# Optimization experiments

Measured on AMD Instinct MI355X. Metric: run time of the kernel, lower is better.

## Reference

```python
import jax, jax.numpy as jnp
import numpy as np

KS = 3      # deformable kernel size
PAD = 1     # module padding


def conv3x3(x, w, b):
    y = jax.lax.conv_general_dilated(
        x, w, window_strides=(1, 1), padding=((1, 1), (1, 1)),
        dimension_numbers=('NCHW', 'OIHW', 'NCHW'))
    return y + b[None, :, None, None]


def setup_inputs() -> dict:
    key = jax.random.key(0)
    ks = jax.random.split(key, 9)
    B, C, H, W = 4, 64, 128, 128
    f = lambda k, s: jax.random.normal(k, s, dtype=jnp.float32)
    return {
        'feature_size': f(ks[0], (B, C, H, W)),
        'feature_context': f(ks[1], (B, C, H, W)),
        'x': f(ks[2], (B, C, H, W)),
        'p_conv_w': f(ks[3], (2 * KS * KS, C, 3, 3)) * 0.01,
        'p_conv_b': f(ks[4], (2 * KS * KS,)) * 0.01,
        'f_conv_w': f(ks[5], (C * KS * KS, C, 3, 3)) * 0.05,
        'f_conv_b': f(ks[6], (C * KS * KS,)) * 0.05,
        'm_conv_w': f(ks[7], (KS * KS, C, 3, 3)) * 0.01,
        'm_conv_b': f(ks[8], (KS * KS,)) * 0.01,
    }


def reference(feature_size, feature_context, x,
              p_conv_w, p_conv_b, f_conv_w, f_conv_b, m_conv_w, m_conv_b):
    ks = KS
    N = ks * ks
    offset = conv3x3(feature_size, p_conv_w, p_conv_b)            # [B, 2N, H, W]
    psffilter = conv3x3(feature_context, f_conv_w, f_conv_b)      # [B, C*N, H, W]
    m = jax.nn.sigmoid(conv3x3(feature_size, m_conv_w, m_conv_b)) # [B, N, H, W]

    B, C, H, W = x.shape
    xp = jnp.pad(x, ((0, 0), (0, 0), (PAD, PAD), (PAD, PAD)))     # [B, C, H+2, W+2]
    Hp, Wp = xp.shape[2], xp.shape[3]

    # sampling locations p = p0 + pn + offset (coords in padded frame; p0 starts at 1)
    r = jnp.arange(-(ks - 1) // 2, (ks - 1) // 2 + 1, dtype=jnp.float32)
    dx = jnp.repeat(r, ks)        # rows:  [-1,-1,-1, 0,0,0, 1,1,1]
    dy = jnp.tile(r, ks)          # cols:  [-1, 0, 1] * 3
    pn = jnp.concatenate([dx, dy])[None, :, None, None]           # [1, 2N, 1, 1]
    px0 = jnp.arange(1, H + 1, dtype=jnp.float32)[None, None, :, None]
    py0 = jnp.arange(1, W + 1, dtype=jnp.float32)[None, None, None, :]
    p0 = jnp.concatenate([jnp.broadcast_to(px0, (1, N, H, W)),
                          jnp.broadcast_to(py0, (1, N, H, W))], axis=1)
    p = jnp.transpose(p0 + pn + offset, (0, 2, 3, 1))             # [B, H, W, 2N]
    px, py = p[..., :N], p[..., N:]

    fx, fy = jnp.floor(px), jnp.floor(py)
    ltx = jnp.clip(fx, 0, Hp - 1)
    lty = jnp.clip(fy, 0, Wp - 1)
    rbx = jnp.clip(fx + 1, 0, Hp - 1)
    rby = jnp.clip(fy + 1, 0, Wp - 1)
    pxc = jnp.clip(px, 0, Hp - 1)
    pyc = jnp.clip(py, 0, Wp - 1)

    g_lt = (1 + (ltx - pxc)) * (1 + (lty - pyc))
    g_rb = (1 - (rbx - pxc)) * (1 - (rby - pyc))
    g_lb = (1 + (ltx - pxc)) * (1 - (rby - pyc))
    g_rt = (1 - (rbx - pxc)) * (1 + (lty - pyc))

    ltx_i, lty_i = ltx.astype(jnp.int32), lty.astype(jnp.int32)
    rbx_i, rby_i = rbx.astype(jnp.int32), rby.astype(jnp.int32)

    gather = jax.vmap(lambda xb, ix, iy: xb[:, ix, iy])  # per-batch -> [C, H, W, N]
    x_lt = gather(xp, ltx_i, lty_i)
    x_rb = gather(xp, rbx_i, rby_i)
    x_lb = gather(xp, ltx_i, rby_i)
    x_rt = gather(xp, rbx_i, lty_i)

    x_off = (g_lt[:, None] * x_lt + g_rb[:, None] * x_rb +
             g_lb[:, None] * x_lb + g_rt[:, None] * x_rt)         # [B, C, H, W, N]

    x_off = x_off * jnp.transpose(m, (0, 2, 3, 1))[:, None]       # modulation

    # _reshape_x_offset: [B,C,H,W,ks,ks] -> [B,C,H*ks,W*ks]
    x_off = x_off.reshape(B, C, H, W, ks, ks)
    x_off = x_off.transpose(0, 1, 2, 4, 3, 5).reshape(B, C, H * ks, W * ks)

    # FAC: unfold(kernel=ks, stride=ks, pad=(ks-1)//2) then per-pixel filter mult-sum
    pad = (ks - 1) // 2
    xf = jnp.pad(x_off, ((0, 0), (0, 0), (pad, pad), (pad, pad)))
    xf = xf[:, :, :H * ks, :W * ks].reshape(B, C, H, ks, W, ks)
    xf = xf.transpose(0, 2, 4, 1, 3, 5).reshape(B, H, W, C, ks * ks)   # [B,H,W,C,9]
    weight = jnp.transpose(psffilter, (0, 2, 3, 1)).reshape(B, H, W, C, ks * ks)
    out = jnp.einsum('bhwck,bhwck->bchw', xf, weight)
    return out
```

## Files before the change

kernel.cpp:

```cpp
#include <hip/hip_runtime.h>

typedef __bf16 bf16;
typedef __bf16 bf16x8 __attribute__((ext_vector_type(8)));
typedef unsigned short u16x8 __attribute__((ext_vector_type(8)));
typedef float f32x4 __attribute__((ext_vector_type(4)));
typedef int i32x4 __attribute__((ext_vector_type(4)));

#define HH 128
#define WW 128
#define HP 130

__global__ __launch_bounds__(256) void zero_rings(
    bf16* __restrict__ fs_t, bf16* __restrict__ ctx_t, float* __restrict__ xp) {
  const int idx = blockIdx.x * 256 + threadIdx.x;
  const f32x4 z = {0.f, 0.f, 0.f, 0.f};
  int r, chunk;
  char* base;
  if (idx < 33024) {
    chunk = idx & 7;
    int cell = idx >> 3;
    r = cell % 516;
    int bb = cell / 516;
    int b = bb & 3;
    bf16* out = (bb >> 2) ? ctx_t : fs_t;
    int row, col;
    if (r < 130)      { row = 0;   col = r; }
    else if (r < 260) { row = 129; col = r - 130; }
    else { int s = r - 260; row = 1 + (s >> 1); col = (s & 1) ? 129 : 0; }
    base = (char*)(out + ((size_t)(b * HP + row) * HP + col) * 64);
  } else {
    int i2 = idx - 33024;
    chunk = i2 & 15;
    int cell = i2 >> 4;
    r = cell % 516;
    int b = cell / 516;
    int row, col;
    if (r < 130)      { row = 0;   col = r; }
    else if (r < 260) { row = 129; col = r - 130; }
    else { int s = r - 260; row = 1 + (s >> 1); col = (s & 1) ? 129 : 0; }
    base = (char*)(xp + ((size_t)(b * HP + row) * HP + col) * 64);
  }
  *reinterpret_cast<f32x4*>(base + chunk * 16) = z;
}

__global__ __launch_bounds__(256) void transpose_all(
    const float* __restrict__ fs, const float* __restrict__ ctx,
    const float* __restrict__ x, bf16* __restrict__ fs_t,
    bf16* __restrict__ ctx_t, float* __restrict__ xp) {
  __shared__ float tile[64][65];
  const int z = blockIdx.z;
  const int b = z & 3, which = z >> 2;
  const float* in = which == 0 ? fs : (which == 1 ? ctx : x);
  const int y = blockIdx.y, x0 = blockIdx.x * 64;
  const int tid = threadIdx.x;
#pragma unroll
  for (int pass = 0; pass < 16; ++pass) {
    int ci = pass * 4 + (tid >> 6), xx = tid & 63;
    tile[ci][xx] = in[((b * 64 + ci) * HH + y) * WW + x0 + xx];
  }
  __syncthreads();
  if (which == 2) {
#pragma unroll
    for (int pass = 0; pass < 16; ++pass) {
      int xx = pass * 4 + (tid >> 6), ci = tid & 63;
      xp[((size_t)(b * HP + y + 1) * HP + (x0 + xx + 1)) * 64 + ci] = tile[ci][xx];
    }
  } else {
    bf16* out = which ? ctx_t : fs_t;
#pragma unroll
    for (int pass = 0; pass < 16; ++pass) {
      int xx = pass * 4 + (tid >> 6), ci = tid & 63;
      out[((size_t)(b * HP + y + 1) * HP + (x0 + xx + 1)) * 64 + ci] = (bf16)tile[ci][xx];
    }
  }
}

__global__ void build_bfrag(const float* __restrict__ fw,
                            const float* __restrict__ pw,
                            const float* __restrict__ mw,
                            bf16* __restrict__ dstPsf,
                            bf16* __restrict__ dstOffm) {
  if ((int)blockIdx.x < 162) {
    int idx = blockIdx.x * 256 + threadIdx.x;
    int lane = idx & 63;
    int nt = (idx >> 6) % 9;
    int kc = ((idx >> 6) / 9) % 18;
    int cc = (idx >> 6) / 162;
    int np = cc * 144 + nt * 16 + (lane & 15);
    int n = (np & 63) * 9 + (np >> 6);
    int q = lane >> 4;
    bf16x8 v;
#pragma unroll
    for (int j = 0; j < 8; ++j) {
      int k = kc * 32 + q * 8 + j;
      int tap = k >> 6, ci = k & 63;
      v[j] = (bf16)fw[(n * 64 + ci) * 9 + tap];
    }
    *reinterpret_cast<bf16x8*>(dstPsf + (size_t)idx * 8) = v;
  } else {
    int idx = (blockIdx.x - 162) * 256 + threadIdx.x;
    int lane = idx & 63;
    int nt = (idx >> 6) & 1;
    int kc = (idx >> 6) >> 1;
    int n = nt * 16 + (lane & 15);
    int q = lane >> 4;
    bf16x8 v;
#pragma unroll
    for (int j = 0; j < 8; ++j) {
      int k = kc * 32 + q * 8 + j;
      int tap = k >> 6, ci = k & 63;
      float w = 0.f;
      if (n < 18) w = pw[(n * 64 + ci) * 9 + tap];
      else if (n < 27) w = mw[((n - 18) * 64 + ci) * 9 + tap];
      v[j] = (bf16)w;
    }
    *reinterpret_cast<bf16x8*>(dstOffm + (size_t)idx * 8) = v;
  }
}

__global__ __launch_bounds__(512, 4) void conv_mega(
    const bf16* __restrict__ ctx_t, const bf16* __restrict__ fs_t,
    const bf16* __restrict__ Bf, const bf16* __restrict__ Bf2,
    const float* __restrict__ fb, const float* __restrict__ pb,
    const float* __restrict__ mb, bf16* __restrict__ Pg,
    float* __restrict__ OM, int b0, int offmN) {
  __shared__ __align__(16) char smem[78336];
  ushort* apatch = (ushort*)smem;
  const int tid = threadIdx.x;
  const int lane = tid & 63, wv = tid >> 6;
  const int q = lane >> 4, col = lane & 15;
  const int bid = blockIdx.x;

  if ((int)bid < offmN) {
    const int b = bid >> 6, t = bid & 63;
    const int h0 = (t >> 3) * 16, w0 = (t & 7) * 16;
    const ushort* Atu = (const ushort*)fs_t;
#pragma unroll
    for (int it = 0; it < 6; ++it) {
      int flat = it * 512 + tid;
      if (flat < 2592) {
        int px = flat >> 3, c8 = flat & 7;
        int py = px / 18, pxx = px - py * 18;
        u16x8 v = *(const u16x8*)(Atu + ((size_t)((b * HP + h0 + py) * HP + (w0 + pxx))) * 64 + c8 * 8);
        *(u16x8*)(apatch + px * 64 + ((c8 ^ (px & 7)) * 8)) = v;
      }
    }
    __syncthreads();
    f32x4 acc[2][2];
#pragma unroll
    for (int s = 0; s < 2; ++s) {
      acc[s][0] = (f32x4){0.f, 0.f, 0.f, 0.f};
      acc[s][1] = (f32x4){0.f, 0.f, 0.f, 0.f};
    }
    const bf16* bl = Bf2 + lane * 8;
#pragma unroll
    for (int dh = 0; dh < 3; ++dh)
#pragma unroll
      for (int dw = 0; dw < 3; ++dw) {
        const int tap = dh * 3 + dw;
        bf16x8 a[2][2];
#pragma unroll
        for (int s = 0; s < 2; ++s) {
          int p = (s * 8 + wv + dh) * 18 + (col + dw);
#pragma unroll
          for (int hf = 0; hf < 2; ++hf) {
            int ch = (hf * 4 + q) ^ (p & 7);
            a[s][hf] = *(const bf16x8*)((const bf16*)apatch + p * 64 + ch * 8);
          }
        }
#pragma unroll
        for (int hf = 0; hf < 2; ++hf)
#pragma unroll
          for (int nt = 0; nt < 2; ++nt) {
            bf16x8 bb = *(const bf16x8*)(bl + (size_t)(((tap * 2 + hf) * 2 + nt) * 512));
#pragma unroll
            for (int s = 0; s < 2; ++s)
              acc[s][nt] = __builtin_amdgcn_mfma_f32_16x16x32_bf16(a[s][hf], bb, acc[s][nt], 0, 0, 0);
          }
      }
    float* OMb = OM + (size_t)b * 16384 * 32;
#pragma unroll
    for (int nt = 0; nt < 2; ++nt) {
      int n = nt * 16 + col;
#pragma unroll
      for (int s = 0; s < 2; ++s) {
        int h = h0 + s * 8 + wv;
#pragma unroll
        for (int j = 0; j < 4; ++j) {
          int w = w0 + q * 4 + j;
          float v = acc[s][nt][j];
          float r;
          if (n < 18) r = v + pb[n];
          else if (n < 27) { float z = v + mb[n - 18]; r = 1.f / (1.f + __expf(-z)); }
          else r = 0.f;
          OMb[(size_t)(h * WW + w) * 32 + n] = r;
        }
      }
    }
    return;
  }

  const int pid = bid - offmN;
  const int cc = pid & 3;
  const int rest = pid >> 2;
  const int brel = rest >> 6;
  const int b = b0 + brel;
  const int t = rest & 63;
  const int h0 = (t >> 3) * 16, w0 = (t & 7) * 16;
  char* BsmBase = smem + 41472;
  const char* BfC = (const char*)Bf + (size_t)cc * 165888;

  {
    const char* gs = BfC;
#pragma unroll
    for (int it = 0; it < 3; ++it) {
      int flat = it * 512 + wv * 64;
      if (flat < 1152) {
        __builtin_amdgcn_global_load_lds(
            (const __attribute__((address_space(1))) void*)(gs + (size_t)(flat + lane) * 16),
            (__attribute__((address_space(3))) void*)(BsmBase + flat * 16), 16, 0, 0);
      }
    }
  }

  const ushort* Atu = (const ushort*)ctx_t;
#pragma unroll
  for (int it = 0; it < 6; ++it) {
    int flat = it * 512 + tid;
    if (flat < 2592) {
      int px = flat >> 3, c8 = flat & 7;
      int py = px / 18, pxx = px - py * 18;
      u16x8 v = *(const u16x8*)(Atu + ((size_t)((b * HP + h0 + py) * HP + (w0 + pxx))) * 64 + c8 * 8);
      *(u16x8*)(apatch + px * 64 + ((c8 ^ (px & 7)) * 8)) = v;
    }
  }
  __syncthreads();

  f32x4 acc[2][9];
#pragma unroll
  for (int s = 0; s < 2; ++s)
#pragma unroll
    for (int n = 0; n < 9; ++n) acc[s][n] = (f32x4){0.f, 0.f, 0.f, 0.f};

  for (int tap = 0; tap < 9; ++tap) {
    const int cur = tap & 1;
    if (tap < 8) {
      const char* gs = BfC + (tap + 1) * 18432;
      char* ld = BsmBase + (cur ^ 1) * 18432;
#pragma unroll
      for (int it = 0; it < 3; ++it) {
        int flat = it * 512 + wv * 64;
        if (flat < 1152) {
          __builtin_amdgcn_global_load_lds(
              (const __attribute__((address_space(1))) void*)(gs + (size_t)(flat + lane) * 16),
              (__attribute__((address_space(3))) void*)(ld + flat * 16), 16, 0, 0);
        }
      }
    }

    const int dh = tap >= 6 ? 2 : (tap >= 3 ? 1 : 0);
    const int dw = tap - dh * 3;
    bf16x8 a[2][2];
#pragma unroll
    for (int s = 0; s < 2; ++s) {
      int p = (s * 8 + wv + dh) * 18 + (col + dw);
#pragma unroll
      for (int hf = 0; hf < 2; ++hf) {
        int ch = (hf * 4 + q) ^ (p & 7);
        a[s][hf] = *(const bf16x8*)((const bf16*)apatch + p * 64 + ch * 8);
      }
    }
    const bf16* Bsm = (const bf16*)(BsmBase + cur * 18432);
#pragma unroll
    for (int hf = 0; hf < 2; ++hf) {
      const bf16* bp = Bsm + (size_t)(hf * 9) * 512 + lane * 8;
#pragma unroll
      for (int nt = 0; nt < 9; ++nt) {
        bf16x8 bb = *(const bf16x8*)(bp + nt * 512);
#pragma unroll
        for (int s = 0; s < 2; ++s)
          acc[s][nt] = __builtin_amdgcn_mfma_f32_16x16x32_bf16(a[s][hf], bb, acc[s][nt], 0, 0, 0);
      }
    }
    __syncthreads();
  }

  bf16* Pp = Pg + (size_t)brel * 16384 * 576;
#pragma unroll
  for (int nt = 0; nt < 9; ++nt) {
    int np = cc * 144 + nt * 16 + col;
    float bias = fb[(np & 63) * 9 + (np >> 6)];
#pragma unroll
    for (int s = 0; s < 2; ++s) {
      int h = h0 + s * 8 + wv;
#pragma unroll
      for (int j = 0; j < 4; ++j) {
        int w = w0 + q * 4 + j;
        Pp[(size_t)(h * WW + w) * 576 + np] = (bf16)(acc[s][nt][j] + bias);
      }
    }
  }
}

__global__ __launch_bounds__(256, 4) void sampler(
    const bf16* __restrict__ Pg, const float* __restrict__ xp,
    const float* __restrict__ OM, float* __restrict__ out, int b0) {
  __shared__ float smem[64][21];
  __shared__ __align__(16) float wts[144][4];
  __shared__ __align__(16) int   offs[144][4];
  const int tid = threadIdx.x;
  const int wv = tid >> 6, c = tid & 63;
  const int blk = blockIdx.x;
  const int brel = blk >> 10;
  const int b = b0 + brel;
  const int h = (blk >> 3) & 127;
  const int w0 = (blk & 7) * 16;

  const float* xpb = xp + (size_t)b * (HP * HP * 64) + c;
  const float* OMb = OM + (size_t)b * 16384 * 32;
  const bf16* Pbase = Pg + ((size_t)brel * 16384 + h * WW + w0) * 576;

  if (tid < 144) {
    const int pl = tid / 9, tap = tid - pl * 9;
    const int i3 = tap / 3, j3 = tap - i3 * 3;
    const int dh = (i3 == 0) ? -1 : 0, ri = (i3 == 0) ? 2 : (i3 - 1);
    const int dw = (j3 == 0) ? -1 : 0, rj = (j3 == 0) ? 2 : (j3 - 1);
    const int hh = h + dh, ww2 = w0 + pl + dw;
    f32x4 g = {0.f, 0.f, 0.f, 0.f};
    i32x4 o = {0, 0, 0, 0};
    if (hh >= 0 && ww2 >= 0) {
      const int np = ri * 3 + rj;
      const float* omp = OMb + (size_t)(hh * WW + ww2) * 32;
      float ox = omp[np], oy = omp[9 + np], mv = omp[18 + np];
      float px = (float)(hh + ri) + ox;
      float py = (float)(ww2 + rj) + oy;
      float fx = floorf(px), fy = floorf(py);
      float ltx = fminf(fmaxf(fx, 0.f), 129.f);
      float lty = fminf(fmaxf(fy, 0.f), 129.f);
      float rbx = fminf(fmaxf(fx + 1.f, 0.f), 129.f);
      float rby = fminf(fmaxf(fy + 1.f, 0.f), 129.f);
      float pxc = fminf(fmaxf(px, 0.f), 129.f);
      float pyc = fminf(fmaxf(py, 0.f), 129.f);
      g[0] = (1.f + ltx - pxc) * (1.f + lty - pyc) * mv;
      g[1] = (1.f - rbx + pxc) * (1.f - rby + pyc) * mv;
      g[2] = (1.f + ltx - pxc) * (1.f - rby + pyc) * mv;
      g[3] = (1.f - rbx + pxc) * (1.f + lty - pyc) * mv;
      int ix0 = (int)ltx, iy0 = (int)lty, ix1 = (int)rbx, iy1 = (int)rby;
      o[0] = (ix0 * HP + iy0) * 64;
      o[1] = (ix1 * HP + iy1) * 64;
      o[2] = (ix0 * HP + iy1) * 64;
      o[3] = (ix1 * HP + iy0) * 64;
    }
    *reinterpret_cast<f32x4*>(&wts[tid][0]) = g;
    *reinterpret_cast<i32x4*>(&offs[tid][0]) = o;
  }
  __syncthreads();

#pragma unroll
  for (int k = 0; k < 4; ++k) {
    const int pl = wv * 4 + k;
    const int w = w0 + pl;
    const bf16* Pp = Pbase + (size_t)pl * 576;
    float res = 0.f;
#pragma unroll
    for (int tap = 0; tap < 9; ++tap) {
      const int i3 = tap / 3, j3 = tap - i3 * 3;
      if ((i3 == 0 && h == 0) || (j3 == 0 && w == 0)) continue;
      const int idx = pl * 9 + tap;
      f32x4 g = *reinterpret_cast<const f32x4*>(&wts[idx][0]);
      i32x4 o = *reinterpret_cast<const i32x4*>(&offs[idx][0]);
      float x_lt = xpb[o[0]];
      float x_rb = xpb[o[1]];
      float x_lb = xpb[o[2]];
      float x_rt = xpb[o[3]];
      float sv = g[0] * x_lt + g[1] * x_rb + g[2] * x_lb + g[3] * x_rt;
      float pv = (float)Pp[tap * 64 + c];
      res += pv * sv;
    }
    smem[c][pl] = res;
  }
  __syncthreads();
  const int c2 = tid >> 2;
  const int wi = (tid & 3) * 4;
  f32x4 v;
#pragma unroll
  for (int i = 0; i < 4; ++i) v[i] = smem[c2][wi + i];
  *reinterpret_cast<f32x4*>(out + ((size_t)(b * 64 + c2) * HH + h) * WW + w0 + wi) = v;
}

extern "C" void kernel_launch(void* const* d_in, const int* in_sizes, int n_in,
                              void* d_out, int out_size, void* d_ws, size_t ws_size,
                              hipStream_t stream) {
  (void)in_sizes; (void)n_in; (void)out_size;
  const float* fs  = (const float*)d_in[0];
  const float* ctx = (const float*)d_in[1];
  const float* x   = (const float*)d_in[2];
  const float* pw  = (const float*)d_in[3];
  const float* pb  = (const float*)d_in[4];
  const float* fw  = (const float*)d_in[5];
  const float* fb  = (const float*)d_in[6];
  const float* mw  = (const float*)d_in[7];
  const float* mb  = (const float*)d_in[8];

  char* ws = (char*)d_ws;
  bf16*  ctx_t = (bf16*)(ws);
  bf16*  fs_t  = (bf16*)(ws + 8652800);
  float* xp    = (float*)(ws + 17305600);
  bf16*  Bf    = (bf16*)(ws + 34611200);
  bf16*  Bf2   = (bf16*)(ws + 35274752);
  float* OM    = (float*)(ws + 35311616);
  bf16*  Pg    = (bf16*)(ws + 43700224);

  zero_rings<<<258, 256, 0, stream>>>(fs_t, ctx_t, xp);
  transpose_all<<<dim3(2, 128, 12), 256, 0, stream>>>(fs, ctx, x, fs_t, ctx_t, xp);
  build_bfrag<<<171, 256, 0, stream>>>(fw, pw, mw, Bf, Bf2);

  const size_t need4 = 43700224 + 4ull * 18874368;
  if (ws_size >= need4) {
    conv_mega<<<1280, 512, 0, stream>>>(ctx_t, fs_t, Bf, Bf2, fb, pb, mb, Pg, OM, 0, 256);
    sampler<<<4096, 256, 0, stream>>>(Pg, xp, OM, (float*)d_out, 0);
  } else {
    conv_mega<<<768, 512, 0, stream>>>(ctx_t, fs_t, Bf, Bf2, fb, pb, mb, Pg, OM, 0, 256);
    sampler<<<2048, 256, 0, stream>>>(Pg, xp, OM, (float*)d_out, 0);
    conv_mega<<<512, 512, 0, stream>>>(ctx_t, fs_t, Bf, Bf2, fb, pb, mb, Pg, OM, 2, 0);
    sampler<<<2048, 256, 0, stream>>>(Pg, xp, OM, (float*)d_out, 2);
  }
}
```

Baseline: 190.0 us.

## Merge prep kernels into one launch and retile conv MFMA warp work 4x5

Three small preprocessing kernels (ring zeroing, transpose, B-fragment build) are folded into one launch whose block index selects the role, removing two launch gaps. In the main conv kernel, each wave now covers 4 pixel rows by 5 (or 4) N-tiles instead of 2 rows by all 9 N-tiles. This gives more A-fragment reuse per B load and fewer LDS B reads per MFMA. The accumulator footprint rises from 18 to 20 tiles, so launch bounds drop to 3 blocks per CU. The N split is uneven across wave groups, 5 vs 4 tiles, which leaves some imbalance.

```diff
diff --git a/kernel.cpp b/kernel.cpp
--- a/kernel.cpp
+++ b/kernel.cpp
@@ -10,78 +10,81 @@
 #define WW 128
 #define HP 130
 
-__global__ __launch_bounds__(256) void zero_rings(
-    bf16* __restrict__ fs_t, bf16* __restrict__ ctx_t, float* __restrict__ xp) {
-  const int idx = blockIdx.x * 256 + threadIdx.x;
-  const f32x4 z = {0.f, 0.f, 0.f, 0.f};
-  int r, chunk;
-  char* base;
-  if (idx < 33024) {
-    chunk = idx & 7;
-    int cell = idx >> 3;
-    r = cell % 516;
-    int bb = cell / 516;
-    int b = bb & 3;
-    bf16* out = (bb >> 2) ? ctx_t : fs_t;
-    int row, col;
-    if (r < 130)      { row = 0;   col = r; }
-    else if (r < 260) { row = 129; col = r - 130; }
-    else { int s = r - 260; row = 1 + (s >> 1); col = (s & 1) ? 129 : 0; }
-    base = (char*)(out + ((size_t)(b * HP + row) * HP + col) * 64);
-  } else {
-    int i2 = idx - 33024;
-    chunk = i2 & 15;
-    int cell = i2 >> 4;
-    r = cell % 516;
-    int b = cell / 516;
-    int row, col;
-    if (r < 130)      { row = 0;   col = r; }
-    else if (r < 260) { row = 129; col = r - 130; }
-    else { int s = r - 260; row = 1 + (s >> 1); col = (s & 1) ? 129 : 0; }
-    base = (char*)(xp + ((size_t)(b * HP + row) * HP + col) * 64);
-  }
-  *reinterpret_cast<f32x4*>(base + chunk * 16) = z;
-}
-
-__global__ __launch_bounds__(256) void transpose_all(
+__global__ __launch_bounds__(256) void prep(
     const float* __restrict__ fs, const float* __restrict__ ctx,
-    const float* __restrict__ x, bf16* __restrict__ fs_t,
-    bf16* __restrict__ ctx_t, float* __restrict__ xp) {
+    const float* __restrict__ x, const float* __restrict__ fw,
+    const float* __restrict__ pw, const float* __restrict__ mw,
+    bf16* __restrict__ fs_t, bf16* __restrict__ ctx_t, float* __restrict__ xp,
+    bf16* __restrict__ dstPsf, bf16* __restrict__ dstOffm) {
   __shared__ float tile[64][65];
-  const int z = blockIdx.z;
-  const int b = z & 3, which = z >> 2;
-  const float* in = which == 0 ? fs : (which == 1 ? ctx : x);
-  const int y = blockIdx.y, x0 = blockIdx.x * 64;
+  const int bid = blockIdx.x;
   const int tid = threadIdx.x;
-#pragma unroll
-  for (int pass = 0; pass < 16; ++pass) {
-    int ci = pass * 4 + (tid >> 6), xx = tid & 63;
-    tile[ci][xx] = in[((b * 64 + ci) * HH + y) * WW + x0 + xx];
-  }
-  __syncthreads();
-  if (which == 2) {
+
+  if (bid < 258) {
+    const int idx = bid * 256 + tid;
+    const f32x4 z = {0.f, 0.f, 0.f, 0.f};
+    int r, chunk;
+    char* base;
+    if (idx < 33024) {
+      chunk = idx & 7;
+      int cell = idx >> 3;
+      r = cell % 516;
+      int bb = cell / 516;
+      int b = bb & 3;
+      bf16* out = (bb >> 2) ? ctx_t : fs_t;
+      int row, col;
+      if (r < 130)      { row = 0;   col = r; }
+      else if (r < 260) { row = 129; col = r - 130; }
+      else { int s = r - 260; row = 1 + (s >> 1); col = (s & 1) ? 129 : 0; }
+      base = (char*)(out + ((size_t)(b * HP + row) * HP + col) * 64);
+    } else {
+      int i2 = idx - 33024;
+      chunk = i2 & 15;
+      int cell = i2 >> 4;
+      r = cell % 516;
+      int b = cell / 516;
+      int row, col;
+      if (r < 130)      { row = 0;   col = r; }
+      else if (r < 260) { row = 129; col = r - 130; }
+      else { int s = r - 260; row = 1 + (s >> 1); col = (s & 1) ? 129 : 0; }
+      base = (char*)(xp + ((size_t)(b * HP + row) * HP + col) * 64);
+    }
+    *reinterpret_cast<f32x4*>(base + chunk * 16) = z;
+    return;
+  }
+
+  if (bid < 3330) {
+    const int t = bid - 258;
+    const int bx = t & 1, by = (t >> 1) & 127, bz = t >> 8;
+    const int b = bz & 3, which = bz >> 2;
+    const float* in = which == 0 ? fs : (which == 1 ? ctx : x);
+    const int y = by, x0 = bx * 64;
 #pragma unroll
     for (int pass = 0; pass < 16; ++pass) {
-      int xx = pass * 4 + (tid >> 6), ci = tid & 63;
-      xp[((size_t)(b * HP + y + 1) * HP + (x0 + xx + 1)) * 64 + ci] = tile[ci][xx];
-    }
-  } else {
-    bf16* out = which ? ctx_t : fs_t;
-#pragma unroll
-    for (int pass = 0; pass < 16; ++pass) {
-      int xx = pass * 4 + (tid >> 6), ci = tid & 63;
-      out[((size_t)(b * HP + y + 1) * HP + (x0 + xx + 1)) * 64 + ci] = (bf16)tile[ci][xx];
-    }
-  }
-}
-
-__global__ void build_bfrag(const float* __restrict__ fw,
-                            const float* __restrict__ pw,
-                            const float* __restrict__ mw,
-                            bf16* __restrict__ dstPsf,
-                            bf16* __restrict__ dstOffm) {
-  if ((int)blockIdx.x < 162) {
-    int idx = blockIdx.x * 256 + threadIdx.x;
+      int ci = pass * 4 + (tid >> 6), xx = tid & 63;
+      tile[ci][xx] = in[((b * 64 + ci) * HH + y) * WW + x0 + xx];
+    }
+    __syncthreads();
+    if (which == 2) {
+#pragma unroll
+      for (int pass = 0; pass < 16; ++pass) {
+        int xx = pass * 4 + (tid >> 6), ci = tid & 63;
+        xp[((size_t)(b * HP + y + 1) * HP + (x0 + xx + 1)) * 64 + ci] = tile[ci][xx];
+      }
+    } else {
+      bf16* out = which ? ctx_t : fs_t;
+#pragma unroll
+      for (int pass = 0; pass < 16; ++pass) {
+        int xx = pass * 4 + (tid >> 6), ci = tid & 63;
+        out[((size_t)(b * HP + y + 1) * HP + (x0 + xx + 1)) * 64 + ci] = (bf16)tile[ci][xx];
+      }
+    }
+    return;
+  }
+
+  const int bx = bid - 3330;
+  if (bx < 162) {
+    int idx = bx * 256 + tid;
     int lane = idx & 63;
     int nt = (idx >> 6) % 9;
     int kc = ((idx >> 6) / 9) % 18;
@@ -98,7 +101,7 @@
     }
     *reinterpret_cast<bf16x8*>(dstPsf + (size_t)idx * 8) = v;
   } else {
-    int idx = (blockIdx.x - 162) * 256 + threadIdx.x;
+    int idx = (bx - 162) * 256 + tid;
     int lane = idx & 63;
     int nt = (idx >> 6) & 1;
     int kc = (idx >> 6) >> 1;
@@ -118,7 +121,7 @@
   }
 }
 
-__global__ __launch_bounds__(512, 4) void conv_mega(
+__global__ __launch_bounds__(512, 3) void conv_mega(
     const bf16* __restrict__ ctx_t, const bf16* __restrict__ fs_t,
     const bf16* __restrict__ Bf, const bf16* __restrict__ Bf2,
     const float* __restrict__ fb, const float* __restrict__ pb,
@@ -207,6 +210,7 @@
   const int b = b0 + brel;
   const int t = rest & 63;
   const int h0 = (t >> 3) * 16, w0 = (t & 7) * 16;
+  const int sg = wv & 3, ng = wv >> 2;
   char* BsmBase = smem + 41472;
   const char* BfC = (const char*)Bf + (size_t)cc * 165888;
 
@@ -236,11 +240,11 @@
   }
   __syncthreads();
 
-  f32x4 acc[2][9];
-#pragma unroll
-  for (int s = 0; s < 2; ++s)
-#pragma unroll
-    for (int n = 0; n < 9; ++n) acc[s][n] = (f32x4){0.f, 0.f, 0.f, 0.f};
+  f32x4 acc[4][5];
+#pragma unroll
+  for (int s = 0; s < 4; ++s)
+#pragma unroll
+    for (int n = 0; n < 5; ++n) acc[s][n] = (f32x4){0.f, 0.f, 0.f, 0.f};
 
   for (int tap = 0; tap < 9; ++tap) {
     const int cur = tap & 1;
@@ -260,10 +264,10 @@
 
     const int dh = tap >= 6 ? 2 : (tap >= 3 ? 1 : 0);
     const int dw = tap - dh * 3;
-    bf16x8 a[2][2];
-#pragma unroll
-    for (int s = 0; s < 2; ++s) {
-      int p = (s * 8 + wv + dh) * 18 + (col + dw);
+    bf16x8 a[4][2];
+#pragma unroll
+    for (int s = 0; s < 4; ++s) {
+      int p = (sg * 4 + s + dh) * 18 + (col + dw);
 #pragma unroll
       for (int hf = 0; hf < 2; ++hf) {
         int ch = (hf * 4 + q) ^ (p & 7);
@@ -273,12 +277,13 @@
     const bf16* Bsm = (const bf16*)(BsmBase + cur * 18432);
 #pragma unroll
     for (int hf = 0; hf < 2; ++hf) {
-      const bf16* bp = Bsm + (size_t)(hf * 9) * 512 + lane * 8;
-#pragma unroll
-      for (int nt = 0; nt < 9; ++nt) {
-        bf16x8 bb = *(const bf16x8*)(bp + nt * 512);
-#pragma unroll
-        for (int s = 0; s < 2; ++s)
+#pragma unroll
+      for (int nt = 0; nt < 5; ++nt) {
+        if (ng && nt == 4) continue;
+        const int ntg = ng * 5 + nt;
+        bf16x8 bb = *(const bf16x8*)(Bsm + (size_t)(hf * 9 + ntg) * 512 + lane * 8);
+#pragma unroll
+        for (int s = 0; s < 4; ++s)
           acc[s][nt] = __builtin_amdgcn_mfma_f32_16x16x32_bf16(a[s][hf], bb, acc[s][nt], 0, 0, 0);
       }
     }
@@ -287,12 +292,14 @@
 
   bf16* Pp = Pg + (size_t)brel * 16384 * 576;
 #pragma unroll
-  for (int nt = 0; nt < 9; ++nt) {
-    int np = cc * 144 + nt * 16 + col;
+  for (int nt = 0; nt < 5; ++nt) {
+    if (ng && nt == 4) continue;
+    const int ntg = ng * 5 + nt;
+    int np = cc * 144 + ntg * 16 + col;
     float bias = fb[(np & 63) * 9 + (np >> 6)];
 #pragma unroll
-    for (int s = 0; s < 2; ++s) {
-      int h = h0 + s * 8 + wv;
+    for (int s = 0; s < 4; ++s) {
+      int h = h0 + sg * 4 + s;
 #pragma unroll
       for (int j = 0; j < 4; ++j) {
         int w = w0 + q * 4 + j;
@@ -411,9 +418,8 @@
   float* OM    = (float*)(ws + 35311616);
   bf16*  Pg    = (bf16*)(ws + 43700224);
 
-  zero_rings<<<258, 256, 0, stream>>>(fs_t, ctx_t, xp);
-  transpose_all<<<dim3(2, 128, 12), 256, 0, stream>>>(fs, ctx, x, fs_t, ctx_t, xp);
-  build_bfrag<<<171, 256, 0, stream>>>(fw, pw, mw, Bf, Bf2);
+  prep<<<3501, 256, 0, stream>>>(fs, ctx, x, fw, pw, mw,
+                                 fs_t, ctx_t, xp, Bf, Bf2);
 
   const size_t need4 = 43700224 + 4ull * 18874368;
   if (ws_size >= need4) {
```

After: 246.6 us. 29.8% more time.
